# Optimization experiments

Hardware: AMD Instinct MI355X
Metric: run time of the kernel (lower is better)

The kernel has to match this reference:

```python
import jax, jax.numpy as jnp
import numpy as np

B, S = 32, 2048
E = int(S * 3.0)  # MLP expansion = 6144
NEG_SLOPE = 0.5
LN_EPS = 1e-5
RENORM_EPS = 2.220446049250313e-16  # torch.finfo(float).eps (float64)
N_ATTN, N_MLP = 2, 2  # layers 0,2 attn; 1,3 mlp


def setup_inputs() -> dict:
    key = jax.random.key(0)
    ks = jax.random.split(key, 14)
    s = 0.05
    return {
        "x": jax.random.normal(ks[0], (B, S), dtype=jnp.float32),
        # AttentionBlock params (stacked over 2 attn layers)
        "attn_ln_g": jnp.ones((N_ATTN, S), jnp.float32),
        "attn_ln_b": jnp.zeros((N_ATTN, S), jnp.float32),
        "in_proj_w": jax.random.normal(ks[1], (N_ATTN, 3), jnp.float32) * s,  # q,k,v scalar weights (embed_dim=1)
        "in_proj_b": jax.random.normal(ks[2], (N_ATTN, 3), jnp.float32) * s,
        "out_w": jax.random.normal(ks[3], (N_ATTN,), jnp.float32) * s,
        "out_b": jax.random.normal(ks[4], (N_ATTN,), jnp.float32) * s,
        # MLP params (stacked over 2 mlp layers); torch Linear layout [out,in]
        "mlp_ln_g": jnp.ones((N_MLP, S), jnp.float32),
        "mlp_ln_b": jnp.zeros((N_MLP, S), jnp.float32),
        "W1": jax.random.normal(ks[5], (N_MLP, E, S), jnp.float32) * (1.0 / np.sqrt(S)),
        "b1": jax.random.normal(ks[6], (N_MLP, E), jnp.float32) * s,
        "W2": jax.random.normal(ks[7], (N_MLP, S, E), jnp.float32) * (1.0 / np.sqrt(E)),
        "b2": jax.random.normal(ks[8], (N_MLP, S), jnp.float32) * s,
    }


def _layernorm(x, g, b):
    mu = jnp.mean(x, axis=-1, keepdims=True)
    v = jnp.mean(jnp.square(x - mu), axis=-1, keepdims=True)  # biased, as nn.LayerNorm
    return (x - mu) * jax.lax.rsqrt(v + LN_EPS) * g + b


def _attn_block(x, g, b, ipw, ipb, ow, ob):
    u = _layernorm(x, g, b)                      # [B,S]
    q = u * ipw[0] + ipb[0]
    k = u * ipw[1] + ipb[1]
    v = u * ipw[2] + ipb[2]
    # embed_dim=1, head_dim=1 -> scale = 1/sqrt(1) = 1
    scores = jnp.einsum('bi,bj->bij', q, k)      # [B,S,S]
    a = jax.nn.softmax(scores, axis=-1)
    o = jnp.einsum('bij,bj->bi', a, v)           # [B,S]
    o = o * ow + ob                              # out_proj (1x1)
    return o + x


def _mlp_block(x, g, b, W1, b1, W2, b2):
    u = _layernorm(x, g, b)
    h = u @ W1.T + b1                            # [B,E]
    h = jnp.where(h >= 0, h, NEG_SLOPE * h)      # LeakyReLU(0.5)
    h = h @ W2.T + b2                            # [B,S]
    return h + x


def reference(x, attn_ln_g, attn_ln_b, in_proj_w, in_proj_b, out_w, out_b,
              mlp_ln_g, mlp_ln_b, W1, b1, W2, b2):
    mean0 = jnp.mean(x, axis=1, keepdims=True)
    var0 = jnp.var(x, axis=1, ddof=1, keepdims=True)  # torch.var unbiased
    for i in range(N_ATTN):  # layer order: attn, mlp, attn, mlp
        x = _attn_block(x, attn_ln_g[i], attn_ln_b[i], in_proj_w[i], in_proj_b[i], out_w[i], out_b[i])
        x = _mlp_block(x, mlp_ln_g[i], mlp_ln_b[i], W1[i], b1[i], W2[i], b2[i])
    m = jnp.mean(x, axis=1, keepdims=True)
    v = jnp.var(x, axis=1, ddof=1, keepdims=True)
    x = (x - m) / jnp.sqrt(v + RENORM_EPS)
    x = x * jnp.sqrt(var0 + RENORM_EPS) + mean0
    return x
```

## Files before the change

kernel.cpp:

```cpp
#include <hip/hip_runtime.h>
#include <math.h>

#define BB 32
#define SS 2048
#define EE 6144
#define KS2 12
#define NCH 4

typedef __bf16 bf16x8 __attribute__((ext_vector_type(8)));
typedef float f32x16 __attribute__((ext_vector_type(16)));
typedef float f32x4 __attribute__((ext_vector_type(4)));

__global__ __launch_bounds__(512) void k_attn(const float* __restrict__ xin,
                                              float* __restrict__ xout,
                                              const float* __restrict__ g,
                                              const float* __restrict__ be,
                                              const float* __restrict__ ipw,
                                              const float* __restrict__ ipb,
                                              const float* __restrict__ owp,
                                              const float* __restrict__ obp,
                                              float* __restrict__ stats,
                                              const float* __restrict__ mlpPart,
                                              const float* __restrict__ b2,
                                              float* __restrict__ pstat) {
  int b = blockIdx.y;
  const float* xrow = xin + b * SS;
  __shared__ float rowbuf[SS];
  __shared__ float2 uv[SS];
  __shared__ float red[16], red2[16], redP[8];
  __shared__ float smu, srs, sqc, sqw, skm;
  __shared__ float ldsS[8][NCH], ldsT[8][NCH];
  __shared__ float bcS[NCH], bcT[NCH];
  int tid = threadIdx.x;
  int lane = tid & 63, wid = tid >> 6;

  const float CN[NCH] = { 0.92387953f,  0.38268343f, -0.38268343f, -0.92387953f};
  const float WN[NCH] = { 0.38268343f, -0.92387953f,  0.92387953f, -0.38268343f};

  float s, s2;
  {
    float4* rb4 = reinterpret_cast<float4*>(rowbuf);
    const float4* xr4 = reinterpret_cast<const float4*>(xrow);
    float4 o;
    if (mlpPart) {
      const float4* b24 = reinterpret_cast<const float4*>(b2);
      float4 xv = xr4[tid];
      float4 bv = b24[tid];
      float4 pv[KS2];
#pragma unroll
      for (int ks = 0; ks < KS2; ks++)
        pv[ks] = reinterpret_cast<const float4*>(mlpPart + (size_t)ks * (32 * SS) + (size_t)b * SS)[tid];
      o.x = xv.x + bv.x; o.y = xv.y + bv.y; o.z = xv.z + bv.z; o.w = xv.w + bv.w;
#pragma unroll
      for (int ks = 0; ks < KS2; ks++) {
        o.x += pv[ks].x; o.y += pv[ks].y; o.z += pv[ks].z; o.w += pv[ks].w;
      }
      rb4[tid] = o;
    } else {
      o = xr4[tid];
      rb4[tid] = o;
    }
    s = (o.x + o.y) + (o.z + o.w);
    s2 = fmaf(o.x, o.x, fmaf(o.y, o.y, fmaf(o.z, o.z, o.w * o.w)));
  }
  for (int off = 32; off; off >>= 1) { s += __shfl_down(s, off); s2 += __shfl_down(s2, off); }
  if (lane == 0) { red[wid] = s; red[8 + wid] = s2; }
  __syncthreads();
  if (tid == 0) {
    float ts = 0.f, ts2 = 0.f;
#pragma unroll
    for (int w = 0; w < 8; w++) { ts += red[w]; ts2 += red[8 + w]; }
    float mu = ts / SS;
    float var = ts2 / SS - mu * mu;
    smu = mu; srs = rsqrtf(var + 1e-5f);
    if (stats && blockIdx.x == 0) {
      stats[b] = mu;
      stats[BB + b] = (ts2 - SS * mu * mu) / (SS - 1);
    }
  }
  __syncthreads();
  float mu = smu, rs = srs;
  float wq = ipw[0], wk = ipw[1], wv = ipw[2];
  float bq = ipb[0], bk = ipb[1], bv = ipb[2];

  float umax = -1e30f, umin = 1e30f;
  for (int j = tid; j < SS; j += 512) {
    float u = (rowbuf[j] - mu) * rs * g[j] + be[j];
    uv[j] = make_float2(u, fmaf(u, wv, bv));
    umax = fmaxf(umax, u);
    umin = fminf(umin, u);
  }
  for (int off = 32; off; off >>= 1) {
    umax = fmaxf(umax, __shfl_down(umax, off));
    umin = fminf(umin, __shfl_down(umin, off));
  }
  if (lane == 0) { red2[wid] = umax; red2[8 + wid] = umin; }
  __syncthreads();
  if (tid == 0) {
    float ux = -1e30f, un = 1e30f;
#pragma unroll
    for (int w = 0; w < 8; w++) { ux = fmaxf(ux, red2[w]); un = fminf(un, red2[8 + w]); }
    float ka = fmaf(ux, wk, bk), kb = fmaf(un, wk, bk);
    skm = 0.5f * (ka + kb);
    float qa = fmaf(ux, wq, bq), qb2 = fmaf(un, wq, bq);
    float qlo = fminf(qa, qb2), qhi = fmaxf(qa, qb2);
    sqc = 0.5f * (qlo + qhi);
    sqw = fmaxf(0.5f * (qhi - qlo), 1e-12f);
  }
  __syncthreads();
  float qc = sqc, qw = sqw, km = skm;

  const float L2E = 1.4426950408889634f;
  float qn[NCH], an[NCH];
#pragma unroll
  for (int n = 0; n < NCH; n++) {
    qn[n] = fmaf(qw, CN[n], qc);
    an[n] = L2E * qn[n];
  }

  float Sa[NCH], Ta[NCH];
#pragma unroll
  for (int n = 0; n < NCH; n++) { Sa[n] = 0.f; Ta[n] = 0.f; }
  for (int j = tid; j < SS; j += 512) {
    float2 c = uv[j];
    float kd = fmaf(c.x, wk, bk) - km;
#pragma unroll
    for (int n = 0; n < NCH; n++) {
      float e = __builtin_amdgcn_exp2f(an[n] * kd);
      Sa[n] += e;
      Ta[n] = fmaf(e, c.y, Ta[n]);
    }
  }
#pragma unroll
  for (int n = 0; n < NCH; n++) {
    for (int off = 32; off; off >>= 1) {
      Sa[n] += __shfl_down(Sa[n], off);
      Ta[n] += __shfl_down(Ta[n], off);
    }
  }
  if (lane == 0) {
#pragma unroll
    for (int n = 0; n < NCH; n++) { ldsS[wid][n] = Sa[n]; ldsT[wid][n] = Ta[n]; }
  }
  __syncthreads();
  if (tid < NCH) {
    float ss = 0.f, tt = 0.f;
#pragma unroll
    for (int w = 0; w < 8; w++) { ss += ldsS[w][tid]; tt += ldsT[w][tid]; }
    bcS[tid] = ss; bcT[tid] = tt;
  }
  __syncthreads();

  float po = 0.f, po2 = 0.f;
  if (tid < 256) {
    int i = (blockIdx.x << 8) + tid;
    float u = uv[i].x;
    float q = fmaf(u, wq, bq);
    float tiny = qw * 1e-10f;
    float num = 0.f, den = 0.f;
#pragma unroll
    for (int n = 0; n < NCH; n++) {
      float d = q - qn[n];
      d = copysignf(fmaxf(fabsf(d), tiny), d);
      float cc = WN[n] / d;
      num = fmaf(cc, bcT[n], num);
      den = fmaf(cc, bcS[n], den);
    }
    float ov = fmaf(num / den, owp[0], obp[0]) + rowbuf[i];
    xout[b * SS + i] = ov;
    po = ov;
    po2 = ov * ov;
  }
  for (int off = 32; off; off >>= 1) {
    po += __shfl_down(po, off);
    po2 += __shfl_down(po2, off);
  }
  if (lane == 0 && wid < 4) { redP[wid] = po; redP[4 + wid] = po2; }
  __syncthreads();
  if (tid == 0) {
    pstat[blockIdx.x * BB + b] = (redP[0] + redP[1]) + (redP[2] + redP[3]);
    pstat[8 * BB + blockIdx.x * BB + b] = (redP[4] + redP[5]) + (redP[6] + redP[7]);
  }
}

__global__ __launch_bounds__(256) void k_ln_bf(const float* __restrict__ x,
                                               const float* __restrict__ pstat,
                                               const float* __restrict__ g,
                                               const float* __restrict__ be,
                                               __bf16* __restrict__ ubf) {
  int b = blockIdx.x;
  const float* row = x + b * SS;
  float s = 0.f, s2 = 0.f;
#pragma unroll
  for (int c = 0; c < 8; c++) {
    s += pstat[c * BB + b];
    s2 += pstat[8 * BB + c * BB + b];
  }
  float mu = s * (1.f / SS);
  float var = s2 * (1.f / SS) - mu * mu;
  float rs = rsqrtf(var + 1e-5f);
  int t = threadIdx.x;
  float4 v0 = *reinterpret_cast<const float4*>(row + t * 8);
  float4 v1 = *reinterpret_cast<const float4*>(row + t * 8 + 4);
  float4 g0 = *reinterpret_cast<const float4*>(g + t * 8);
  float4 g1 = *reinterpret_cast<const float4*>(g + t * 8 + 4);
  float4 b0 = *reinterpret_cast<const float4*>(be + t * 8);
  float4 b1 = *reinterpret_cast<const float4*>(be + t * 8 + 4);
  bf16x8 o;
  o[0] = (__bf16)((v0.x - mu) * rs * g0.x + b0.x);
  o[1] = (__bf16)((v0.y - mu) * rs * g0.y + b0.y);
  o[2] = (__bf16)((v0.z - mu) * rs * g0.z + b0.z);
  o[3] = (__bf16)((v0.w - mu) * rs * g0.w + b0.w);
  o[4] = (__bf16)((v1.x - mu) * rs * g1.x + b1.x);
  o[5] = (__bf16)((v1.y - mu) * rs * g1.y + b1.y);
  o[6] = (__bf16)((v1.z - mu) * rs * g1.z + b1.z);
  o[7] = (__bf16)((v1.w - mu) * rs * g1.w + b1.w);
  *reinterpret_cast<bf16x8*>(ubf + t * 256 + b * 8) = o;
}

__device__ __forceinline__ void gemm_chunk(const float* __restrict__ wp,
                                           const __bf16* __restrict__ up,
                                           f32x16& acc) {
  bf16x8 ub[8];
  f32x4 wa[8], wb2[8];
#pragma unroll
  for (int t = 0; t < 8; ++t) ub[t] = *reinterpret_cast<const bf16x8*>(up + (t << 9));
#pragma unroll
  for (int t = 0; t < 4; ++t) {
    wa[2 * t]     = *reinterpret_cast<const f32x4*>(wp + (t << 4));
    wa[2 * t + 1] = *reinterpret_cast<const f32x4*>(wp + (t << 4) + 4);
  }
#pragma unroll
  for (int t = 4; t < 8; ++t) {
    wb2[2 * (t - 4)]     = *reinterpret_cast<const f32x4*>(wp + (t << 4));
    wb2[2 * (t - 4) + 1] = *reinterpret_cast<const f32x4*>(wp + (t << 4) + 4);
  }
#pragma unroll
  for (int t = 0; t < 4; ++t) {
    bf16x8 av;
    av[0] = (__bf16)wa[2 * t][0];     av[1] = (__bf16)wa[2 * t][1];
    av[2] = (__bf16)wa[2 * t][2];     av[3] = (__bf16)wa[2 * t][3];
    av[4] = (__bf16)wa[2 * t + 1][0]; av[5] = (__bf16)wa[2 * t + 1][1];
    av[6] = (__bf16)wa[2 * t + 1][2]; av[7] = (__bf16)wa[2 * t + 1][3];
    acc = __builtin_amdgcn_mfma_f32_32x32x16_bf16(av, ub[t], acc, 0, 0, 0);
  }
#pragma unroll
  for (int t = 0; t < 4; ++t) {
    bf16x8 av;
    av[0] = (__bf16)wb2[2 * t][0];     av[1] = (__bf16)wb2[2 * t][1];
    av[2] = (__bf16)wb2[2 * t][2];     av[3] = (__bf16)wb2[2 * t][3];
    av[4] = (__bf16)wb2[2 * t + 1][0]; av[5] = (__bf16)wb2[2 * t + 1][1];
    av[6] = (__bf16)wb2[2 * t + 1][2]; av[7] = (__bf16)wb2[2 * t + 1][3];
    acc = __builtin_amdgcn_mfma_f32_32x32x16_bf16(av, ub[4 + t], acc, 0, 0, 0);
  }
}

__global__ __launch_bounds__(256, 4) void k_gemm1(const __bf16* __restrict__ Ubf,
                                                  const float* __restrict__ W,
                                                  const float* __restrict__ bias,
                                                  __bf16* __restrict__ hbf) {
  __shared__ float ls[3][16][64];
  __shared__ float st[32][33];
  int tid = threadIdx.x;
  int w = tid >> 6, lane = tid & 63;
  int l31 = lane & 31, h = lane >> 5;
  int e0 = blockIdx.x << 5;

  f32x16 acc = {0.f, 0.f, 0.f, 0.f, 0.f, 0.f, 0.f, 0.f,
                0.f, 0.f, 0.f, 0.f, 0.f, 0.f, 0.f, 0.f};
#pragma unroll
  for (int c = 0; c < 4; ++c) {
    int kc = (w << 9) + (c << 7);
    const float* wp = W + (size_t)(e0 + l31) * SS + kc + (h << 3);
    const __bf16* up = Ubf + (size_t)((kc >> 3) + h) * 256 + (l31 << 3);
    gemm_chunk(wp, up, acc);
  }

  if (w) {
#pragma unroll
    for (int r = 0; r < 16; ++r) ls[w - 1][r][lane] = acc[r];
  }
  __syncthreads();
  if (w == 0) {
#pragma unroll
    for (int r = 0; r < 16; ++r) {
      float v = acc[r] + ls[0][r][lane] + ls[1][r][lane] + ls[2][r][lane];
      int row = (r & 3) + ((r >> 2) << 3) + (h << 2);
      st[row][l31] = v;
    }
  }
  __syncthreads();
  if (tid < 128) {
    int eg = tid >> 5, b = tid & 31;
    bf16x8 o;
#pragma unroll
    for (int j = 0; j < 8; j++) {
      float v = st[eg * 8 + j][b] + bias[e0 + eg * 8 + j];
      o[j] = (__bf16)(v >= 0.f ? v : 0.5f * v);
    }
    *reinterpret_cast<bf16x8*>(hbf + (size_t)((e0 >> 3) + eg) * 256 + b * 8) = o;
  }
}

__global__ __launch_bounds__(256, 4) void k_gemm2(const __bf16* __restrict__ Ubf,
                                                  const float* __restrict__ W,
                                                  float* __restrict__ part,
                                                  int K) {
  __shared__ float ls[3][16][64];
  __shared__ float st[32][33];
  int tid = threadIdx.x;
  int w = tid >> 6, lane = tid & 63;
  int l31 = lane & 31, h = lane >> 5;
  int s0 = blockIdx.x << 5;
  int kc = (blockIdx.y << 9) + (w << 7);
  const float* wp = W + (size_t)(s0 + l31) * K + kc + (h << 3);
  const __bf16* up = Ubf + (size_t)((kc >> 3) + h) * 256 + (l31 << 3);

  f32x16 acc = {0.f, 0.f, 0.f, 0.f, 0.f, 0.f, 0.f, 0.f,
                0.f, 0.f, 0.f, 0.f, 0.f, 0.f, 0.f, 0.f};
  gemm_chunk(wp, up, acc);

  if (w) {
#pragma unroll
    for (int r = 0; r < 16; ++r) ls[w - 1][r][lane] = acc[r];
  }
  __syncthreads();
  if (w == 0) {
#pragma unroll
    for (int r = 0; r < 16; ++r) {
      float v = acc[r] + ls[0][r][lane] + ls[1][r][lane] + ls[2][r][lane];
      int row = (r & 3) + ((r >> 2) << 3) + (h << 2);
      st[row][l31] = v;
    }
  }
  __syncthreads();
  {
    float* out = part + (size_t)blockIdx.y * (32 * SS);
    int bb = tid >> 3, i0 = (tid & 7) << 2;
    float4 o4;
    o4.x = st[i0 + 0][bb];
    o4.y = st[i0 + 1][bb];
    o4.z = st[i0 + 2][bb];
    o4.w = st[i0 + 3][bb];
    *reinterpret_cast<float4*>(out + (size_t)bb * SS + s0 + i0) = o4;
  }
}

__global__ __launch_bounds__(256) void k_final(const float* __restrict__ xbuf,
                                               const float* __restrict__ part,
                                               const float* __restrict__ b2,
                                               const float* __restrict__ stats,
                                               float* __restrict__ out) {
  int b = blockIdx.x;
  __shared__ float rowbuf[SS];
  __shared__ float sm[8];
  __shared__ float smu, srs;
  int tid = threadIdx.x;
  float4* rb4 = reinterpret_cast<float4*>(rowbuf);
  const float4* xr4 = reinterpret_cast<const float4*>(xbuf + (size_t)b * SS);
  const float4* b24 = reinterpret_cast<const float4*>(b2);
#pragma unroll
  for (int it = 0; it < 2; ++it) {
    int jj = tid + (it << 8);
    float4 xv = xr4[jj];
    float4 bv = b24[jj];
    float4 pv[KS2];
#pragma unroll
    for (int ks = 0; ks < KS2; ks++)
      pv[ks] = reinterpret_cast<const float4*>(part + (size_t)ks * (32 * SS) + (size_t)b * SS)[jj];
    float4 o;
    o.x = xv.x + bv.x; o.y = xv.y + bv.y; o.z = xv.z + bv.z; o.w = xv.w + bv.w;
#pragma unroll
    for (int ks = 0; ks < KS2; ks++) {
      o.x += pv[ks].x; o.y += pv[ks].y; o.z += pv[ks].z; o.w += pv[ks].w;
    }
    rb4[jj] = o;
  }
  __syncthreads();

  float s = 0.f, s2 = 0.f;
  for (int j = tid; j < SS; j += 256) { float v = rowbuf[j]; s += v; s2 += v * v; }
  for (int off = 32; off; off >>= 1) { s += __shfl_down(s, off); s2 += __shfl_down(s2, off); }
  int lane = tid & 63, wid = tid >> 6;
  if (lane == 0) { sm[wid] = s; sm[4 + wid] = s2; }
  __syncthreads();
  if (tid == 0) {
    float ts = sm[0] + sm[1] + sm[2] + sm[3];
    float ts2 = sm[4] + sm[5] + sm[6] + sm[7];
    float mu = ts / SS;
    float var = (ts2 - SS * mu * mu) / (SS - 1);
    smu = mu;
    srs = rsqrtf(var + 2.220446049250313e-16f);
  }
  __syncthreads();
  float mu = smu, rs = srs;
  float scale = sqrtf(stats[BB + b] + 2.220446049250313e-16f);
  float mean0 = stats[b];
  for (int j = tid; j < SS; j += 256) {
    out[(size_t)b * SS + j] = (rowbuf[j] - mu) * rs * scale + mean0;
  }
}

extern "C" void kernel_launch(void* const* d_in, const int* in_sizes, int n_in,
                              void* d_out, int out_size, void* d_ws, size_t ws_size,
                              hipStream_t stream) {
  const float* x         = (const float*)d_in[0];
  const float* attn_ln_g = (const float*)d_in[1];
  const float* attn_ln_b = (const float*)d_in[2];
  const float* ipw       = (const float*)d_in[3];
  const float* ipb       = (const float*)d_in[4];
  const float* out_w     = (const float*)d_in[5];
  const float* out_b     = (const float*)d_in[6];
  const float* mlp_ln_g  = (const float*)d_in[7];
  const float* mlp_ln_b  = (const float*)d_in[8];
  const float* W1        = (const float*)d_in[9];
  const float* b1        = (const float*)d_in[10];
  const float* W2        = (const float*)d_in[11];
  const float* b2        = (const float*)d_in[12];

  float* ws    = (float*)d_ws;
  float* xA    = ws;
  float* xB    = xA + BB * SS;
  __bf16* ubf  = (__bf16*)(xB + BB * SS);
  __bf16* hbf  = (__bf16*)(xB + BB * SS + 32768);
  float* part  = xB + BB * SS + 32768 + 98304;
  float* stats = part + (size_t)KS2 * 32 * SS;
  float* pstat = stats + 64;

  k_attn<<<dim3(SS / 256, BB), 512, 0, stream>>>(x, xA,
                                                 attn_ln_g, attn_ln_b,
                                                 ipw, ipb, out_w, out_b,
                                                 stats, nullptr, nullptr, pstat);
  k_ln_bf<<<BB, 256, 0, stream>>>(xA, pstat, mlp_ln_g, mlp_ln_b, ubf);
  k_gemm1<<<EE / 32, 256, 0, stream>>>(ubf, W1, b1, hbf);
  k_gemm2<<<dim3(SS / 32, KS2), 256, 0, stream>>>(hbf, W2, part, EE);

  k_attn<<<dim3(SS / 256, BB), 512, 0, stream>>>(xA, xB,
                                                 attn_ln_g + SS, attn_ln_b + SS,
                                                 ipw + 3, ipb + 3, out_w + 1, out_b + 1,
                                                 nullptr, part, b2, pstat);
  k_ln_bf<<<BB, 256, 0, stream>>>(xB, pstat, mlp_ln_g + SS, mlp_ln_b + SS, ubf);
  k_gemm1<<<EE / 32, 256, 0, stream>>>(ubf, W1 + (size_t)EE * SS, b1 + EE, hbf);
  k_gemm2<<<dim3(SS / 32, KS2), 256, 0, stream>>>(hbf, W2 + (size_t)SS * EE, part, EE);

  k_final<<<BB, 256, 0, stream>>>(xB, part, b2 + SS, stats, (float*)d_out);
}
```

Measured before the change: 73.63 us.

## Fold MLP LayerNorm into attention epilogue and GEMM1 via algebraic correction

Removes the separate LayerNorm-to-bf16 kernel. The attention kernel now writes g*x in bf16 directly, and GEMM1 applies the mean and rstd correction afterwards using per-row sums W·g and W·b computed on the fly plus per-batch stats from pstat. This saves one launch and one pass over the activations per MLP layer. In exchange GEMM1 reloads W and also reads g and b to form the extra dot products, which adds VALU work and register pressure, so launch bounds drop to 2 waves. Subtracting mu*G1 after the matmul on un-centered bf16 inputs may also lose precision through cancellation.

```diff
diff --git a/kernel.cpp b/kernel.cpp
--- a/kernel.cpp
+++ b/kernel.cpp
@@ -22,12 +22,15 @@
                                               float* __restrict__ stats,
                                               const float* __restrict__ mlpPart,
                                               const float* __restrict__ b2,
-                                              float* __restrict__ pstat) {
+                                              float* __restrict__ pstat,
+                                              const float* __restrict__ gml,
+                                              __bf16* __restrict__ ubf) {
   int b = blockIdx.y;
   const float* xrow = xin + b * SS;
   __shared__ float rowbuf[SS];
   __shared__ float2 uv[SS];
   __shared__ float red[16], red2[16], redP[8];
+  __shared__ float gxs[256];
   __shared__ float smu, srs, sqc, sqw, skm;
   __shared__ float ldsS[8][NCH], ldsT[8][NCH];
   __shared__ float bcS[NCH], bcT[NCH];
@@ -168,6 +171,7 @@
     }
     float ov = fmaf(num / den, owp[0], obp[0]) + rowbuf[i];
     xout[b * SS + i] = ov;
+    gxs[tid] = gml[i] * ov;
     po = ov;
     po2 = ov * ov;
   }
@@ -181,41 +185,12 @@
     pstat[blockIdx.x * BB + b] = (redP[0] + redP[1]) + (redP[2] + redP[3]);
     pstat[8 * BB + blockIdx.x * BB + b] = (redP[4] + redP[5]) + (redP[6] + redP[7]);
   }
-}
-
-__global__ __launch_bounds__(256) void k_ln_bf(const float* __restrict__ x,
-                                               const float* __restrict__ pstat,
-                                               const float* __restrict__ g,
-                                               const float* __restrict__ be,
-                                               __bf16* __restrict__ ubf) {
-  int b = blockIdx.x;
-  const float* row = x + b * SS;
-  float s = 0.f, s2 = 0.f;
-#pragma unroll
-  for (int c = 0; c < 8; c++) {
-    s += pstat[c * BB + b];
-    s2 += pstat[8 * BB + c * BB + b];
-  }
-  float mu = s * (1.f / SS);
-  float var = s2 * (1.f / SS) - mu * mu;
-  float rs = rsqrtf(var + 1e-5f);
-  int t = threadIdx.x;
-  float4 v0 = *reinterpret_cast<const float4*>(row + t * 8);
-  float4 v1 = *reinterpret_cast<const float4*>(row + t * 8 + 4);
-  float4 g0 = *reinterpret_cast<const float4*>(g + t * 8);
-  float4 g1 = *reinterpret_cast<const float4*>(g + t * 8 + 4);
-  float4 b0 = *reinterpret_cast<const float4*>(be + t * 8);
-  float4 b1 = *reinterpret_cast<const float4*>(be + t * 8 + 4);
-  bf16x8 o;
-  o[0] = (__bf16)((v0.x - mu) * rs * g0.x + b0.x);
-  o[1] = (__bf16)((v0.y - mu) * rs * g0.y + b0.y);
-  o[2] = (__bf16)((v0.z - mu) * rs * g0.z + b0.z);
-  o[3] = (__bf16)((v0.w - mu) * rs * g0.w + b0.w);
-  o[4] = (__bf16)((v1.x - mu) * rs * g1.x + b1.x);
-  o[5] = (__bf16)((v1.y - mu) * rs * g1.y + b1.y);
-  o[6] = (__bf16)((v1.z - mu) * rs * g1.z + b1.z);
-  o[7] = (__bf16)((v1.w - mu) * rs * g1.w + b1.w);
-  *reinterpret_cast<bf16x8*>(ubf + t * 256 + b * 8) = o;
+  if (tid < 32) {
+    bf16x8 o;
+#pragma unroll
+    for (int j = 0; j < 8; j++) o[j] = (__bf16)gxs[tid * 8 + j];
+    *reinterpret_cast<bf16x8*>(ubf + (size_t)((blockIdx.x << 5) + tid) * 256 + b * 8) = o;
+  }
 }
 
 __device__ __forceinline__ void gemm_chunk(const float* __restrict__ wp,
@@ -255,12 +230,17 @@
   }
 }
 
-__global__ __launch_bounds__(256, 4) void k_gemm1(const __bf16* __restrict__ Ubf,
+__global__ __launch_bounds__(256, 2) void k_gemm1(const __bf16* __restrict__ Ubf,
                                                   const float* __restrict__ W,
+                                                  const float* __restrict__ gml,
+                                                  const float* __restrict__ bml,
+                                                  const float* __restrict__ pstat,
                                                   const float* __restrict__ bias,
                                                   __bf16* __restrict__ hbf) {
   __shared__ float ls[3][16][64];
   __shared__ float st[32][33];
+  __shared__ float glw[4][32], blw[4][32];
+  __shared__ float smub[32], srsb[32];
   int tid = threadIdx.x;
   int w = tid >> 6, lane = tid & 63;
   int l31 = lane & 31, h = lane >> 5;
@@ -268,12 +248,43 @@
 
   f32x16 acc = {0.f, 0.f, 0.f, 0.f, 0.f, 0.f, 0.f, 0.f,
                 0.f, 0.f, 0.f, 0.f, 0.f, 0.f, 0.f, 0.f};
+  float gl = 0.f, bl = 0.f;
 #pragma unroll
   for (int c = 0; c < 4; ++c) {
     int kc = (w << 9) + (c << 7);
     const float* wp = W + (size_t)(e0 + l31) * SS + kc + (h << 3);
     const __bf16* up = Ubf + (size_t)((kc >> 3) + h) * 256 + (l31 << 3);
+    const float* gp = gml + kc + (h << 3);
+    const float* bp = bml + kc + (h << 3);
+#pragma unroll
+    for (int t = 0; t < 8; ++t) {
+      f32x4 wv0 = *reinterpret_cast<const f32x4*>(wp + (t << 4));
+      f32x4 wv1 = *reinterpret_cast<const f32x4*>(wp + (t << 4) + 4);
+      f32x4 g0 = *reinterpret_cast<const f32x4*>(gp + (t << 4));
+      f32x4 g1 = *reinterpret_cast<const f32x4*>(gp + (t << 4) + 4);
+      f32x4 b0 = *reinterpret_cast<const f32x4*>(bp + (t << 4));
+      f32x4 b1 = *reinterpret_cast<const f32x4*>(bp + (t << 4) + 4);
+#pragma unroll
+      for (int i = 0; i < 4; ++i) {
+        gl = fmaf(wv0[i], g0[i], gl); gl = fmaf(wv1[i], g1[i], gl);
+        bl = fmaf(wv0[i], b0[i], bl); bl = fmaf(wv1[i], b1[i], bl);
+      }
+    }
     gemm_chunk(wp, up, acc);
+  }
+  gl += __shfl_xor(gl, 32);
+  bl += __shfl_xor(bl, 32);
+  if (h == 0) { glw[w][l31] = gl; blw[w][l31] = bl; }
+  if (tid < 32) {
+    float sb = 0.f, sb2 = 0.f;
+#pragma unroll
+    for (int c = 0; c < 8; c++) {
+      sb += pstat[c * BB + tid];
+      sb2 += pstat[8 * BB + c * BB + tid];
+    }
+    float m = sb * (1.f / SS);
+    smub[tid] = m;
+    srsb[tid] = rsqrtf(sb2 * (1.f / SS) - m * m + 1e-5f);
   }
 
   if (w) {
@@ -292,10 +303,14 @@
   __syncthreads();
   if (tid < 128) {
     int eg = tid >> 5, b = tid & 31;
+    float mub = smub[b], rsb = srsb[b];
     bf16x8 o;
 #pragma unroll
     for (int j = 0; j < 8; j++) {
-      float v = st[eg * 8 + j][b] + bias[e0 + eg * 8 + j];
+      int el = eg * 8 + j;
+      float G1 = (glw[0][el] + glw[1][el]) + (glw[2][el] + glw[3][el]);
+      float B1 = (blw[0][el] + blw[1][el]) + (blw[2][el] + blw[3][el]);
+      float v = rsb * (st[el][b] - mub * G1) + B1 + bias[e0 + el];
       o[j] = (__bf16)(v >= 0.f ? v : 0.5f * v);
     }
     *reinterpret_cast<bf16x8*>(hbf + (size_t)((e0 >> 3) + eg) * 256 + b * 8) = o;
@@ -430,17 +445,18 @@
   k_attn<<<dim3(SS / 256, BB), 512, 0, stream>>>(x, xA,
                                                  attn_ln_g, attn_ln_b,
                                                  ipw, ipb, out_w, out_b,
-                                                 stats, nullptr, nullptr, pstat);
-  k_ln_bf<<<BB, 256, 0, stream>>>(xA, pstat, mlp_ln_g, mlp_ln_b, ubf);
-  k_gemm1<<<EE / 32, 256, 0, stream>>>(ubf, W1, b1, hbf);
+                                                 stats, nullptr, nullptr, pstat,
+                                                 mlp_ln_g, ubf);
+  k_gemm1<<<EE / 32, 256, 0, stream>>>(ubf, W1, mlp_ln_g, mlp_ln_b, pstat, b1, hbf);
   k_gemm2<<<dim3(SS / 32, KS2), 256, 0, stream>>>(hbf, W2, part, EE);
 
   k_attn<<<dim3(SS / 256, BB), 512, 0, stream>>>(xA, xB,
                                                  attn_ln_g + SS, attn_ln_b + SS,
                                                  ipw + 3, ipb + 3, out_w + 1, out_b + 1,
-                                                 nullptr, part, b2, pstat);
-  k_ln_bf<<<BB, 256, 0, stream>>>(xB, pstat, mlp_ln_g + SS, mlp_ln_b + SS, ubf);
-  k_gemm1<<<EE / 32, 256, 0, stream>>>(ubf, W1 + (size_t)EE * SS, b1 + EE, hbf);
+                                                 nullptr, part, b2, pstat,
+                                                 mlp_ln_g + SS, ubf);
+  k_gemm1<<<EE / 32, 256, 0, stream>>>(ubf, W1 + (size_t)EE * SS,
+                                       mlp_ln_g + SS, mlp_ln_b + SS, pstat, b1 + EE, hbf);
   k_gemm2<<<dim3(SS / 32, KS2), 256, 0, stream>>>(hbf, W2 + (size_t)SS * EE, part, EE);
 
   k_final<<<BB, 256, 0, stream>>>(xB, part, b2 + SS, stats, (float*)d_out);
```

Result: slower. 97.75 us (+32.8%).
